# Optimization experiments

Measured on AMD Instinct MI355X. Metric: run time of the kernel, lower is better.

The kernel has to match this reference:

```python
import jax, jax.numpy as jnp
import numpy as np

NEG = -1e8


def lstm_scan(x, lens, Wih, Whh, b):
    # x: [B,S,D], lens: [B] int. PyTorch gate order i,f,g,o. Returns [B,S,H], zero at pad.
    B, S, D = x.shape
    H = Whh.shape[1]
    xs = jnp.swapaxes(x, 0, 1)  # [S,B,D]
    ts = jnp.arange(S)

    def step(carry, inp):
        h, c = carry
        xt, t = inp
        gates = xt @ Wih.T + h @ Whh.T + b  # [B,4H]
        i, f, g, o = jnp.split(gates, 4, axis=-1)
        i, f, o = jax.nn.sigmoid(i), jax.nn.sigmoid(f), jax.nn.sigmoid(o)
        g = jnp.tanh(g)
        c_new = f * c + i * g
        h_new = o * jnp.tanh(c_new)
        valid = (t < lens)[:, None]
        h = jnp.where(valid, h_new, h)
        c = jnp.where(valid, c_new, c)
        out = jnp.where(valid, h_new, 0.0)
        return (h, c), out

    init = (jnp.zeros((B, H), x.dtype), jnp.zeros((B, H), x.dtype))
    _, outs = jax.lax.scan(step, init, (xs, ts))
    return jnp.swapaxes(outs, 0, 1)  # [B,S,H]


def bilstm(x, lens, Wih_f, Whh_f, b_f, Wih_b, Whh_b, b_b):
    # forward direction
    out_f = lstm_scan(x, lens, Wih_f, Whh_f, b_f)
    # backward: reverse the valid prefix per sample (packed-sequence semantics)
    S = x.shape[1]
    t = jnp.arange(S)[None, :]
    idx = jnp.where(t < lens[:, None], lens[:, None] - 1 - t, t)  # [B,S]
    xr = jnp.take_along_axis(x, idx[:, :, None], axis=1)
    out_r = lstm_scan(xr, lens, Wih_b, Whh_b, b_b)
    out_b = jnp.take_along_axis(out_r, idx[:, :, None], axis=1)
    return jnp.concatenate([out_f, out_b], axis=-1)


def tnet_forward(seqs_id, seqs_len, asps_len, asps_mask, sent_mask,
                 embed, Wih_f, Whh_f, b_f, Wih_b, Whh_b, b_b,
                 W_cpt, b_cpt, W_as, b_as, Wq, bq, Wk, bk, Wv, bv, Wd, bd):
    seqs = embed[seqs_id]                                   # [B,S,D] (dropout = eval identity)
    seqs_lstm = bilstm(seqs, seqs_len, Wih_f, Whh_f, b_f, Wih_b, Whh_b, b_b)  # [B,S,D]

    # ragged aspect gather + pad + mean == masked mean (asps_mask==0 marks aspect tokens)
    asp_sel = (asps_mask == 0).astype(seqs_lstm.dtype)       # [B,S]
    asps = (seqs_lstm * asp_sel[:, :, None]).sum(axis=1) / asps_len[:, None].astype(seqs_lstm.dtype)
    asps = asps[:, None, :]                                  # [B,1,D]

    # CPT layers (flag='AS'); Attentions = dot-product attn, out = softmax(QK^T + mask) @ K
    x = seqs_lstm
    for _ in range(2):
        score = jax.nn.softmax(jnp.einsum('bqd,bkd->bqk', x, seqs_lstm) + asps_mask[:, None, :], axis=-1)
        attn_out = jnp.einsum('bqk,bkd->bqd', score, seqs_lstm)
        combine = jnp.concatenate([attn_out, x], axis=-1)    # [B,S,2D]
        linear_out = jax.nn.relu(combine @ W_cpt.T + b_cpt)
        scale = jax.nn.sigmoid(x @ W_as.T + b_as)
        x = scale * linear_out + (1.0 - scale) * x

    # QKVAttention over sentence
    D = x.shape[-1]
    Qp = asps @ Wq.T + bq                                    # [B,1,D]
    Kp = x @ Wk.T + bk                                       # [B,S,D]
    Vp = x @ Wv.T + bv
    sc = jax.nn.softmax(jnp.einsum('bqd,bkd->bqk', Qp, Kp) / jnp.sqrt(jnp.asarray(D, x.dtype))
                        + sent_mask[:, None, :], axis=-1)    # [B,1,S]
    out = jnp.einsum('bqk,bkd->bqd', sc, Vp)                 # [B,1,D]
    logits = out[:, 0] @ Wd.T + bd                           # [B,n_class]
    return logits, sc[:, 0]


def setup_inputs() -> dict:
    B, S, V, D, H, NC = 64, 256, 30000, 512, 256, 3
    key = jax.random.key(0)
    ks = jax.random.split(key, 24)

    seqs_id = jax.random.randint(ks[0], (B, S), 0, V)
    seqs_len = jax.random.randint(ks[1], (B,), S // 2, S + 1)
    asps_len = jax.random.randint(ks[2], (B,), 1, 6)
    start = jax.random.randint(ks[3], (B,), 0, S // 2 - 8)   # aspect span inside valid prefix
    pos = jnp.arange(S)[None, :]
    in_span = (pos >= start[:, None]) & (pos < (start + asps_len)[:, None])
    asps_mask = jnp.where(in_span, 0.0, NEG).astype(jnp.float32)
    sent_mask = jnp.where(pos < seqs_len[:, None], 0.0, NEG).astype(jnp.float32)

    def nrm(k, shape, s=0.02):
        return (s * jax.random.normal(k, shape)).astype(jnp.float32)

    inp = dict(seqs_id=seqs_id, seqs_len=seqs_len, asps_len=asps_len,
               asps_mask=asps_mask, sent_mask=sent_mask,
               embed=nrm(ks[4], (V, D), 0.1),
               Wih_f=nrm(ks[5], (4 * H, D)), Whh_f=nrm(ks[6], (4 * H, H)), b_f=jnp.zeros((4 * H,), jnp.float32),
               Wih_b=nrm(ks[7], (4 * H, D)), Whh_b=nrm(ks[8], (4 * H, H)), b_b=jnp.zeros((4 * H,), jnp.float32),
               W_cpt=nrm(ks[9], (D, 2 * D)), b_cpt=jnp.zeros((D,), jnp.float32),
               W_as=nrm(ks[10], (D, D)), b_as=jnp.zeros((D,), jnp.float32),
               Wq=nrm(ks[11], (D, D)), bq=jnp.zeros((D,), jnp.float32),
               Wk=nrm(ks[12], (D, D)), bk=jnp.zeros((D,), jnp.float32),
               Wv=nrm(ks[13], (D, D)), bv=jnp.zeros((D,), jnp.float32),
               Wd=nrm(ks[14], (NC, D)), bd=jnp.zeros((NC,), jnp.float32))
    return inp


def reference(seqs_id, seqs_len, asps_len, asps_mask, sent_mask,
              embed, Wih_f, Whh_f, b_f, Wih_b, Whh_b, b_b,
              W_cpt, b_cpt, W_as, b_as, Wq, bq, Wk, bk, Wv, bv, Wd, bd):
    return tnet_forward(seqs_id, seqs_len, asps_len, asps_mask, sent_mask,
                        embed, Wih_f, Whh_f, b_f, Wih_b, Whh_b, b_b,
                        W_cpt, b_cpt, W_as, b_as, Wq, bq, Wk, bk, Wv, bv, Wd, bd)
```

## Files before the change

### kernel.cpp

```cpp
#include <hip/hip_runtime.h>
#include <math.h>

constexpr int B_ = 64, S_ = 256, D_ = 512, H_ = 256, NC_ = 3;
constexpr int BS = B_ * S_;
constexpr int G4 = 4 * H_;

typedef __attribute__((ext_vector_type(4))) float f32x4;
typedef __attribute__((ext_vector_type(8))) short s16x8;
typedef unsigned short u16;
typedef unsigned long long u64;

template<int ACT>
static __device__ __forceinline__ float activate(float v) {
  if constexpr (ACT == 1) return v > 0.f ? v : 0.f;
  else if constexpr (ACT == 2) return 1.f / (1.f + expf(-v));
  else return v;
}

static __device__ __forceinline__ u16 f2bf_rne(float f) {
  unsigned u = __float_as_uint(f);
  return (u16)((u + 0x7FFFu + ((u >> 16) & 1u)) >> 16);
}
static __device__ __forceinline__ float bf2f(u16 h) {
  return __uint_as_float(((unsigned)h) << 16);
}
static __device__ __forceinline__ void splitf(float f, u16& h, u16& l) {
  h = f2bf_rne(f);
  float r = f - bf2f(h);
  l = f2bf_rne(r);
}

__global__ __launch_bounds__(256) void split_w(
    const float* __restrict__ src, u16* __restrict__ h, u16* __restrict__ l, int n4)
{
  int i = blockIdx.x * 256 + threadIdx.x;
  if (i >= n4) return;
  float4 v = ((const float4*)src)[i];
  ushort4 hh, ll;
  splitf(v.x, hh.x, ll.x); splitf(v.y, hh.y, ll.y);
  splitf(v.z, hh.z, ll.z); splitf(v.w, hh.w, ll.w);
  ((ushort4*)h)[i] = hh;
  ((ushort4*)l)[i] = ll;
}

__global__ __launch_bounds__(256) void gather_split(
    const float* __restrict__ embed, const int* __restrict__ gidx,
    u16* __restrict__ h, u16* __restrict__ l)
{
  int i = blockIdx.x * 256 + threadIdx.x;
  if (i >= BS * D_ / 4) return;
  int r = i >> 7;
  int c = (i & 127) << 2;
  float4 v = *(const float4*)(embed + (size_t)gidx[r] * D_ + c);
  ushort4 hh, ll;
  splitf(v.x, hh.x, ll.x); splitf(v.y, hh.y, ll.y);
  splitf(v.z, hh.z, ll.z); splitf(v.w, hh.w, ll.w);
  ((ushort4*)h)[i] = hh;
  ((ushort4*)l)[i] = ll;
}

template<int ACT, bool BT, bool ADDC, bool ASPL, bool BSPL, bool OSPL>
__global__ __launch_bounds__(256) void mgemm(
    const float* __restrict__ Af, const u16* __restrict__ Ah, const u16* __restrict__ Al,
    const float* __restrict__ Bf, const u16* __restrict__ Bh, const u16* __restrict__ Bl,
    const float* __restrict__ bias, const float* __restrict__ Cin,
    float* __restrict__ Co, u16* __restrict__ Oh, u16* __restrict__ Ol,
    int M, int N, int K, int ldb, long sA, long sB, long sC)
{
  __shared__ u16 AH[128][40];
  __shared__ u16 AL[128][40];
  __shared__ u16 BH[128][40];
  __shared__ u16 BL[128][40];

  const int tid = threadIdx.x;
  const int w = tid >> 6, l = tid & 63;
  const int m0 = blockIdx.x * 128, n0 = blockIdx.y * 128;
  const long zA = (long)blockIdx.z * sA;
  const long zB = (long)blockIdx.z * sB;
  const long zC = (long)blockIdx.z * sC;

  f32x4 acc[2][8];
  #pragma unroll
  for (int i = 0; i < 2; ++i)
    #pragma unroll
    for (int j = 0; j < 8; ++j) acc[i][j] = (f32x4){0.f, 0.f, 0.f, 0.f};

  const int ar = tid >> 1, ahh = tid & 1;
  const int bk = tid >> 3, bnq = tid & 7;
  const int lr = l & 15, lk = (l >> 4) * 8;

  for (int kt = 0; kt < K; kt += 32) {
    {
      int m = m0 + ar;
      if constexpr (ASPL) {
        s16x8 h0 = (s16x8)0, h1 = (s16x8)0, l0 = (s16x8)0, l1 = (s16x8)0;
        if (m < M) {
          const u16* ph = Ah + zA + (size_t)m * K + kt + ahh * 16;
          const u16* pl = Al + zA + (size_t)m * K + kt + ahh * 16;
          h0 = *(const s16x8*)ph; h1 = *(const s16x8*)(ph + 8);
          l0 = *(const s16x8*)pl; l1 = *(const s16x8*)(pl + 8);
        }
        *(s16x8*)&AH[ar][ahh * 16] = h0; *(s16x8*)&AH[ar][ahh * 16 + 8] = h1;
        *(s16x8*)&AL[ar][ahh * 16] = l0; *(s16x8*)&AL[ar][ahh * 16 + 8] = l1;
      } else {
        float vv[16];
        if (m < M) {
          const float* pf = Af + zA + (size_t)m * K + kt + ahh * 16;
          #pragma unroll
          for (int c = 0; c < 4; ++c) {
            float4 v = ((const float4*)pf)[c];
            vv[c * 4] = v.x; vv[c * 4 + 1] = v.y; vv[c * 4 + 2] = v.z; vv[c * 4 + 3] = v.w;
          }
        } else {
          #pragma unroll
          for (int c = 0; c < 16; ++c) vv[c] = 0.f;
        }
        u16 hh[16], ll[16];
        #pragma unroll
        for (int c = 0; c < 16; ++c) splitf(vv[c], hh[c], ll[c]);
        *(s16x8*)&AH[ar][ahh * 16] = *(s16x8*)&hh[0];
        *(s16x8*)&AH[ar][ahh * 16 + 8] = *(s16x8*)&hh[8];
        *(s16x8*)&AL[ar][ahh * 16] = *(s16x8*)&ll[0];
        *(s16x8*)&AL[ar][ahh * 16 + 8] = *(s16x8*)&ll[8];
      }
    }
    if constexpr (BT) {
      if constexpr (BSPL) {
        const u16* ph = Bh + zB + (size_t)(n0 + ar) * ldb + kt + ahh * 16;
        const u16* pl = Bl + zB + (size_t)(n0 + ar) * ldb + kt + ahh * 16;
        *(s16x8*)&BH[ar][ahh * 16] = *(const s16x8*)ph;
        *(s16x8*)&BH[ar][ahh * 16 + 8] = *(const s16x8*)(ph + 8);
        *(s16x8*)&BL[ar][ahh * 16] = *(const s16x8*)pl;
        *(s16x8*)&BL[ar][ahh * 16 + 8] = *(const s16x8*)(pl + 8);
      } else {
        const float* pf = Bf + zB + (size_t)(n0 + ar) * ldb + kt + ahh * 16;
        float vv[16];
        #pragma unroll
        for (int c = 0; c < 4; ++c) {
          float4 v = ((const float4*)pf)[c];
          vv[c * 4] = v.x; vv[c * 4 + 1] = v.y; vv[c * 4 + 2] = v.z; vv[c * 4 + 3] = v.w;
        }
        u16 hh[16], ll[16];
        #pragma unroll
        for (int c = 0; c < 16; ++c) splitf(vv[c], hh[c], ll[c]);
        *(s16x8*)&BH[ar][ahh * 16] = *(s16x8*)&hh[0];
        *(s16x8*)&BH[ar][ahh * 16 + 8] = *(s16x8*)&hh[8];
        *(s16x8*)&BL[ar][ahh * 16] = *(s16x8*)&ll[0];
        *(s16x8*)&BL[ar][ahh * 16 + 8] = *(s16x8*)&ll[8];
      }
    } else {
      const u16* ph = Bh + zB + (size_t)(kt + bk) * ldb + n0 + bnq * 16;
      const u16* pl = Bl + zB + (size_t)(kt + bk) * ldb + n0 + bnq * 16;
      s16x8 h8a = *(const s16x8*)ph, h8b = *(const s16x8*)(ph + 8);
      s16x8 l8a = *(const s16x8*)pl, l8b = *(const s16x8*)(pl + 8);
      #pragma unroll
      for (int jj = 0; jj < 8; ++jj) {
        BH[bnq * 16 + jj][bk] = (u16)h8a[jj];
        BH[bnq * 16 + 8 + jj][bk] = (u16)h8b[jj];
        BL[bnq * 16 + jj][bk] = (u16)l8a[jj];
        BL[bnq * 16 + 8 + jj][bk] = (u16)l8b[jj];
      }
    }
    __syncthreads();

    s16x8 afh[2], afl[2];
    #pragma unroll
    for (int i = 0; i < 2; ++i) {
      afh[i] = *(const s16x8*)&AH[w * 32 + i * 16 + lr][lk];
      afl[i] = *(const s16x8*)&AL[w * 32 + i * 16 + lr][lk];
    }
    #pragma unroll
    for (int j = 0; j < 8; ++j) {
      s16x8 bfh = *(const s16x8*)&BH[j * 16 + lr][lk];
      s16x8 bfl = *(const s16x8*)&BL[j * 16 + lr][lk];
      #pragma unroll
      for (int i = 0; i < 2; ++i) {
        acc[i][j] = __builtin_amdgcn_mfma_f32_16x16x32_bf16(afl[i], bfh, acc[i][j], 0, 0, 0);
        acc[i][j] = __builtin_amdgcn_mfma_f32_16x16x32_bf16(afh[i], bfl, acc[i][j], 0, 0, 0);
        acc[i][j] = __builtin_amdgcn_mfma_f32_16x16x32_bf16(afh[i], bfh, acc[i][j], 0, 0, 0);
      }
    }
    __syncthreads();
  }

  const int rl = (l >> 4) * 4;
  #pragma unroll
  for (int j = 0; j < 8; ++j) {
    int n = n0 + j * 16 + lr;
    float bv = bias ? bias[n] : 0.f;
    #pragma unroll
    for (int i = 0; i < 2; ++i) {
      #pragma unroll
      for (int e = 0; e < 4; ++e) {
        int m = m0 + w * 32 + i * 16 + rl + e;
        if (m < M) {
          float v = acc[i][j][e] + bv;
          if constexpr (ADDC) v += Cin[zC + (size_t)m * N + n];
          v = activate<ACT>(v);
          if constexpr (OSPL) {
            u16 hh, ll; splitf(v, hh, ll);
            Oh[zC + (size_t)m * N + n] = hh;
            Ol[zC + (size_t)m * N + n] = ll;
          } else {
            Co[zC + (size_t)m * N + n] = v;
          }
        }
      }
    }
  }
}

__global__ __launch_bounds__(256) void wf_prep(
    const float* __restrict__ Wf, const float* __restrict__ Wb, u16* __restrict__ WF)
{
  int gid = blockIdx.x * 256 + threadIdx.x;
  int lane = gid & 63;
  int nt = (gid >> 6) & 1;
  int kt = (gid >> 7) & 7;
  int w  = (gid >> 10) & 3;
  int j  = (gid >> 12) & 7;
  int dir = gid >> 15;
  const float* W = dir ? Wb : Wf;
  int r = w * 256 + j * 32 + nt * 16 + (lane & 15);
  int kb = kt * 32 + (lane >> 4) * 8;
  const float* src = W + (size_t)r * H_ + kb;
  u16 hh[8], ll[8];
  #pragma unroll
  for (int c = 0; c < 2; ++c) {
    float4 v = ((const float4*)src)[c];
    splitf(v.x, hh[c*4+0], ll[c*4+0]); splitf(v.y, hh[c*4+1], ll[c*4+1]);
    splitf(v.z, hh[c*4+2], ll[c*4+2]); splitf(v.w, hh[c*4+3], ll[c*4+3]);
  }
  size_t off = (size_t)(gid >> 6) * 1024 + (size_t)lane * 8;
  *(s16x8*)(WF + off)       = *(s16x8*)&hh[0];
  *(s16x8*)(WF + off + 512) = *(s16x8*)&ll[0];
}

__global__ __launch_bounds__(256) void zero_cnt(int* __restrict__ cnt)
{
  int i = blockIdx.x * 256 + threadIdx.x;
  if (i < 8 * 256) cnt[i] = 0;
}

__global__ __launch_bounds__(256, 1) void lstm_dist(
    const float* __restrict__ GX, const u16* __restrict__ WF,
    const int* __restrict__ lens, u16* __restrict__ outH, u16* __restrict__ outL,
    u64* __restrict__ ring64, int* __restrict__ cnt)
{
  const int bid = blockIdx.x;
  const int grp = bid & 7;
  const int j   = bid >> 3;
  const int dir = grp >> 2;
  const int bg  = grp & 3;
  const int b0g = bg * 16;
  const int tid = threadIdx.x;
  const int w = tid >> 6, l = tid & 63;

  const float* gx = GX + (size_t)dir * ((size_t)BS * G4);

  __shared__ int slen[16];
  __shared__ __align__(16) u16 AHs[16][264];
  __shared__ __align__(16) u16 ALs[16][264];
  __shared__ float act[4][16][32];
  if (tid < 16) slen[tid] = lens[b0g + tid];
  __syncthreads();

  s16x8 wh[8][2], wl[8][2];
  #pragma unroll
  for (int kt = 0; kt < 8; ++kt)
    #pragma unroll
    for (int nt = 0; nt < 2; ++nt) {
      size_t q = ((size_t)(((dir * 8 + j) * 4 + w) * 8 + kt) * 2 + nt);
      const u16* p = WF + q * 1024 + (size_t)l * 8;
      wh[kt][nt] = *(const s16x8*)p;
      wl[kt][nt] = *(const s16x8*)(p + 512);
    }

  const int ub = tid >> 4;
  const int uu = (tid & 15) * 2;
  const int len_b = slen[ub];
  float c0s = 0.f, c1s = 0.f, h0s = 0.f, h1s = 0.f;

  int* myCnt = cnt + grp * 256;
  const int lr = l & 15, lkb = (l >> 4) * 8;

  for (int t = 0; t < S_; ++t) {
    float gxv[2][4];
    #pragma unroll
    for (int nt = 0; nt < 2; ++nt)
      #pragma unroll
      for (int e = 0; e < 4; ++e) {
        int b = (l >> 4) * 4 + e;
        int len = slen[b];
        int pos = dir ? (t < len ? len - 1 - t : t) : t;
        gxv[nt][e] = gx[(size_t)((b0g + b) * S_ + pos) * G4 + (w * 256 + j * 32 + nt * 16 + lr)];
      }

    f32x4 acc[2];
    acc[0] = (f32x4){0.f, 0.f, 0.f, 0.f};
    acc[1] = (f32x4){0.f, 0.f, 0.f, 0.f};

    if (t > 0) {
      while (__hip_atomic_load(&myCnt[t - 1], __ATOMIC_RELAXED, __HIP_MEMORY_SCOPE_AGENT) < 32)
        __builtin_amdgcn_s_sleep(1);
      const int slot = (t - 1) & 3;
      const u64* rb = ring64 + ((size_t)slot * 8 + grp) * (16 * 128);
      u64 v[8];
      #pragma unroll
      for (int k = 0; k < 8; ++k)
        v[k] = __hip_atomic_load(&rb[k * 256 + tid], __ATOMIC_RELAXED, __HIP_MEMORY_SCOPE_AGENT);
      #pragma unroll
      for (int k = 0; k < 8; ++k) {
        int idx = k * 256 + tid;
        int b = idx >> 7, p = idx & 127;
        ushort4 q4 = *(ushort4*)&v[k];
        *(unsigned*)&AHs[b][2 * p] = (unsigned)q4.x | ((unsigned)q4.z << 16);
        *(unsigned*)&ALs[b][2 * p] = (unsigned)q4.y | ((unsigned)q4.w << 16);
      }
      __syncthreads();
      #pragma unroll
      for (int kt = 0; kt < 8; ++kt) {
        s16x8 ah = *(const s16x8*)&AHs[lr][kt * 32 + lkb];
        s16x8 al = *(const s16x8*)&ALs[lr][kt * 32 + lkb];
        #pragma unroll
        for (int nt = 0; nt < 2; ++nt) {
          acc[nt] = __builtin_amdgcn_mfma_f32_16x16x32_bf16(al, wh[kt][nt], acc[nt], 0, 0, 0);
          acc[nt] = __builtin_amdgcn_mfma_f32_16x16x32_bf16(ah, wl[kt][nt], acc[nt], 0, 0, 0);
          acc[nt] = __builtin_amdgcn_mfma_f32_16x16x32_bf16(ah, wh[kt][nt], acc[nt], 0, 0, 0);
        }
      }
    }

    #pragma unroll
    for (int nt = 0; nt < 2; ++nt)
      #pragma unroll
      for (int e = 0; e < 4; ++e) {
        float v = acc[nt][e] + gxv[nt][e];
        v = (w == 2) ? tanhf(v) : 1.f / (1.f + expf(-v));
        act[w][(l >> 4) * 4 + e][nt * 16 + lr] = v;
      }
    __syncthreads();

    {
      int pos = dir ? (t < len_b ? len_b - 1 - t : t) : t;
      bool valid = t < len_b;
      float i0 = act[0][ub][uu],     f0 = act[1][ub][uu],     g0 = act[2][ub][uu],     o0 = act[3][ub][uu];
      float i1 = act[0][ub][uu + 1], f1 = act[1][ub][uu + 1], g1 = act[2][ub][uu + 1], o1 = act[3][ub][uu + 1];
      float cn0 = fmaf(f0, c0s, i0 * g0), cn1 = fmaf(f1, c1s, i1 * g1);
      float hn0 = o0 * tanhf(cn0), hn1 = o1 * tanhf(cn1);
      if (valid) { c0s = cn0; h0s = hn0; c1s = cn1; h1s = hn1; }
      ushort4 pk;
      splitf(h0s, pk.x, pk.y); splitf(h1s, pk.z, pk.w);
      const int slot = t & 3;
      size_t ridx = ((size_t)slot * 8 + grp) * (16 * 128) + (size_t)ub * 128 + (j * 32 + uu) / 2;
      __hip_atomic_store(&ring64[ridx], *(u64*)&pk, __ATOMIC_RELAXED, __HIP_MEMORY_SCOPE_AGENT);
      asm volatile("s_waitcnt vmcnt(0)" ::: "memory");
      if (l == 0)
        __hip_atomic_fetch_add(&myCnt[t], 1, __ATOMIC_RELAXED, __HIP_MEMORY_SCOPE_AGENT);
      float ov0 = valid ? hn0 : 0.f, ov1 = valid ? hn1 : 0.f;
      u16 oh0, qq0, oh1, qq1;
      splitf(ov0, oh0, qq0); splitf(ov1, oh1, qq1);
      size_t obase = (size_t)((b0g + ub) * S_ + pos) * (2 * H_) + dir * H_ + j * 32 + uu;
      *(ushort2*)&outH[obase] = make_ushort2(oh0, oh1);
      *(ushort2*)&outL[obase] = make_ushort2(qq0, qq1);
    }
    __syncthreads();
  }
}

__global__ __launch_bounds__(512) void asps_k(
    const u16* __restrict__ lh, const u16* __restrict__ ll,
    const float* __restrict__ amask, const int* __restrict__ alen, float* __restrict__ asps)
{
  int b = blockIdx.x, d = threadIdx.x;
  float acc = 0.f;
  for (int t = 0; t < S_; ++t)
    if (amask[b * S_ + t] == 0.f) {
      size_t i = ((size_t)(b * S_ + t)) * D_ + d;
      acc += bf2f(lh[i]) + bf2f(ll[i]);
    }
  asps[b * D_ + d] = acc / (float)alen[b];
}

__global__ __launch_bounds__(256) void softmax_rows(
    const float* __restrict__ p_, const float* __restrict__ mask,
    u16* __restrict__ ph, u16* __restrict__ pl)
{
  const int row = blockIdx.x;
  const int b = row >> 8;
  const int tid = threadIdx.x;
  const float* p = p_ + (size_t)row * S_;
  float v = p[tid] + mask[(b << 8) | tid];
  float m = v;
  #pragma unroll
  for (int off = 32; off > 0; off >>= 1) m = fmaxf(m, __shfl_xor(m, off));
  __shared__ float r1[4];
  __shared__ float r2[4];
  const int w = tid >> 6, l = tid & 63;
  if (l == 0) r1[w] = m;
  __syncthreads();
  m = fmaxf(fmaxf(r1[0], r1[1]), fmaxf(r1[2], r1[3]));
  float e = expf(v - m);
  float s = e;
  #pragma unroll
  for (int off = 32; off > 0; off >>= 1) s += __shfl_xor(s, off);
  if (l == 0) r2[w] = s;
  __syncthreads();
  s = r2[0] + r2[1] + r2[2] + r2[3];
  float o = e / s;
  u16 hh, ll; splitf(o, hh, ll);
  ph[(size_t)row * S_ + tid] = hh;
  pl[(size_t)row * S_ + tid] = ll;
}

__global__ __launch_bounds__(256) void xupdate(
    const u16* __restrict__ xh, const u16* __restrict__ xl,
    const float4* __restrict__ sc, const float4* __restrict__ lin,
    u16* __restrict__ oh, u16* __restrict__ ol, int n4)
{
  int i = blockIdx.x * 256 + threadIdx.x;
  if (i >= n4) return;
  ushort4 h4 = ((const ushort4*)xh)[i];
  ushort4 l4 = ((const ushort4*)xl)[i];
  float4 s = sc[i], lv = lin[i];
  float x0 = bf2f(h4.x) + bf2f(l4.x);
  float x1 = bf2f(h4.y) + bf2f(l4.y);
  float x2 = bf2f(h4.z) + bf2f(l4.z);
  float x3 = bf2f(h4.w) + bf2f(l4.w);
  float o0 = s.x * lv.x + (1.f - s.x) * x0;
  float o1 = s.y * lv.y + (1.f - s.y) * x1;
  float o2 = s.z * lv.z + (1.f - s.z) * x2;
  float o3 = s.w * lv.w + (1.f - s.w) * x3;
  ushort4 hh, ll;
  splitf(o0, hh.x, ll.x); splitf(o1, hh.y, ll.y);
  splitf(o2, hh.z, ll.z); splitf(o3, hh.w, ll.w);
  ((ushort4*)oh)[i] = hh;
  ((ushort4*)ol)[i] = ll;
}

__global__ __launch_bounds__(256) void final_sc_k(
    const float* __restrict__ Qp, const float* __restrict__ Kp,
    const float* __restrict__ smask, float* __restrict__ outsc)
{
  int b = blockIdx.x, tid = threadIdx.x;
  __shared__ float q[D_];
  q[tid] = Qp[b * D_ + tid];
  q[tid + 256] = Qp[b * D_ + tid + 256];
  __syncthreads();
  const float4* kr = (const float4*)(Kp + ((size_t)(b * S_ + tid)) * D_);
  float acc = 0.f;
  #pragma unroll 4
  for (int d = 0; d < D_ / 4; ++d) {
    float4 kv = kr[d];
    acc += q[4 * d] * kv.x + q[4 * d + 1] * kv.y + q[4 * d + 2] * kv.z + q[4 * d + 3] * kv.w;
  }
  float v = acc / sqrtf((float)D_) + smask[b * S_ + tid];
  float m = v;
  #pragma unroll
  for (int off = 32; off > 0; off >>= 1) m = fmaxf(m, __shfl_xor(m, off));
  __shared__ float r1[4];
  __shared__ float r2[4];
  const int w = tid >> 6, l = tid & 63;
  if (l == 0) r1[w] = m;
  __syncthreads();
  m = fmaxf(fmaxf(r1[0], r1[1]), fmaxf(r1[2], r1[3]));
  float e = expf(v - m);
  float s = e;
  #pragma unroll
  for (int off = 32; off > 0; off >>= 1) s += __shfl_xor(s, off);
  if (l == 0) r2[w] = s;
  __syncthreads();
  s = r2[0] + r2[1] + r2[2] + r2[3];
  outsc[b * S_ + tid] = e / s;
}

__global__ __launch_bounds__(512) void out_vec_k(
    const float* __restrict__ sc, const float* __restrict__ Vp, float* __restrict__ outv)
{
  int b = blockIdx.x, d = threadIdx.x;
  __shared__ float s[S_];
  if (d < S_) s[d] = sc[b * S_ + d];
  __syncthreads();
  float acc = 0.f;
  for (int k = 0; k < S_; ++k) acc = fmaf(s[k], Vp[((size_t)(b * S_ + k)) * D_ + d], acc);
  outv[b * D_ + d] = acc;
}

__global__ __launch_bounds__(192) void logits_k(
    const float* __restrict__ outv, const float* __restrict__ Wd,
    const float* __restrict__ bd, float* __restrict__ out)
{
  int b = blockIdx.x;
  int c = threadIdx.x >> 6, l = threadIdx.x & 63;
  float acc = 0.f;
  for (int d = l; d < D_; d += 64) acc = fmaf(outv[b * D_ + d], Wd[c * D_ + d], acc);
  #pragma unroll
  for (int off = 32; off > 0; off >>= 1) acc += __shfl_down(acc, off);
  if (l == 0) out[b * NC_ + c] = acc + bd[c];
}

extern "C" void kernel_launch(void* const* d_in, const int* in_sizes, int n_in,
                              void* d_out, int out_size, void* d_ws, size_t ws_size,
                              hipStream_t stream)
{
  const int*   seqs_id   = (const int*)d_in[0];
  const int*   seqs_len  = (const int*)d_in[1];
  const int*   asps_len  = (const int*)d_in[2];
  const float* asps_mask = (const float*)d_in[3];
  const float* sent_mask = (const float*)d_in[4];
  const float* embed     = (const float*)d_in[5];
  const float* Wih_f     = (const float*)d_in[6];
  const float* Whh_f     = (const float*)d_in[7];
  const float* b_f       = (const float*)d_in[8];
  const float* Wih_b     = (const float*)d_in[9];
  const float* Whh_b     = (const float*)d_in[10];
  const float* b_b       = (const float*)d_in[11];
  const float* W_cpt     = (const float*)d_in[12];
  const float* b_cpt     = (const float*)d_in[13];
  const float* W_as      = (const float*)d_in[14];
  const float* b_as      = (const float*)d_in[15];
  const float* Wq        = (const float*)d_in[16];
  const float* bq        = (const float*)d_in[17];
  const float* Wk        = (const float*)d_in[18];
  const float* bk        = (const float*)d_in[19];
  const float* Wv        = (const float*)d_in[20];
  const float* bv        = (const float*)d_in[21];
  const float* Wd        = (const float*)d_in[22];
  const float* bd        = (const float*)d_in[23];

  float* w = (float*)d_ws;
  size_t off = 0;
  auto alloc = [&](size_t words) { size_t o = off; off += words; return o; };
  struct Split { u16* h; u16* l; };
  auto salloc = [&](size_t n) {
    size_t o = alloc(n);
    Split s; s.h = (u16*)(w + o); s.l = (u16*)(w + o) + n; return s;
  };

  const size_t off_wf   = alloc(524288);
  const size_t off_ring = alloc(131072);
  const size_t off_cnt  = alloc(2048);
  Split sWihF = salloc(4ul * H_ * D_);
  Split sWihB = salloc(4ul * H_ * D_);
  Split sWcpt = salloc((size_t)D_ * 2 * D_);
  Split sWas  = salloc((size_t)D_ * D_);
  Split sWk   = salloc((size_t)D_ * D_);
  Split sWv   = salloc((size_t)D_ * D_);
  Split sWq   = salloc((size_t)D_ * D_);
  Split sLstm = salloc((size_t)BS * D_);
  const size_t off_asps = alloc((size_t)B_ * D_);
  const size_t off_qp   = alloc((size_t)B_ * D_);
  const size_t off_outv = alloc((size_t)B_ * D_);
  Split sAsps = salloc((size_t)B_ * D_);

  const size_t dyn0 = off;
  Split sXemb; sXemb.h = (u16*)(w + dyn0); sXemb.l = sXemb.h + (size_t)BS * D_;
  float* GX = w + dyn0 + (size_t)BS * D_;
  size_t p2 = dyn0;
  float* scoreF = w + p2;                 p2 += (size_t)B_ * S_ * S_;
  Split sScore; sScore.h = (u16*)(w + p2); sScore.l = sScore.h + (size_t)B_ * S_ * S_; p2 += (size_t)B_ * S_ * S_;
  Split sAttn;  sAttn.h  = (u16*)(w + p2); sAttn.l  = sAttn.h + (size_t)BS * D_;       p2 += (size_t)BS * D_;
  float* lin = w + p2;                    p2 += (size_t)BS * D_;
  float* scl = w + p2;                    p2 += (size_t)BS * D_;
  Split sX;     sX.h     = (u16*)(w + p2); sX.l     = sX.h + (size_t)BS * D_;           p2 += (size_t)BS * D_;

  u16* WF      = (u16*)(w + off_wf);
  u64* ring64  = (u64*)(w + off_ring);
  int* cnt     = (int*)(w + off_cnt);
  float* aspsb = w + off_asps;
  float* qp    = w + off_qp;
  float* outv  = w + off_outv;
  float* Kp    = (float*)sAttn.h;
  float* Vp    = lin;
  float* logits = (float*)d_out;
  float* outsc  = (float*)d_out + B_ * NC_;

  zero_cnt<<<8, 256, 0, stream>>>(cnt);
  wf_prep<<<256, 256, 0, stream>>>(Whh_f, Whh_b, WF);
  split_w<<<512, 256, 0, stream>>>(Wih_f, sWihF.h, sWihF.l, H_ * D_);
  split_w<<<512, 256, 0, stream>>>(Wih_b, sWihB.h, sWihB.l, H_ * D_);
  split_w<<<512, 256, 0, stream>>>(W_cpt, sWcpt.h, sWcpt.l, D_ * 2 * D_ / 4);
  split_w<<<256, 256, 0, stream>>>(W_as, sWas.h, sWas.l, D_ * D_ / 4);
  split_w<<<256, 256, 0, stream>>>(Wk, sWk.h, sWk.l, D_ * D_ / 4);
  split_w<<<256, 256, 0, stream>>>(Wv, sWv.h, sWv.l, D_ * D_ / 4);
  split_w<<<256, 256, 0, stream>>>(Wq, sWq.h, sWq.l, D_ * D_ / 4);
  gather_split<<<BS * D_ / 4 / 256, 256, 0, stream>>>(embed, seqs_id, sXemb.h, sXemb.l);

  mgemm<0, true, false, true, true, false><<<dim3(128, 8, 1), 256, 0, stream>>>(
      nullptr, sXemb.h, sXemb.l, nullptr, sWihF.h, sWihF.l, b_f, nullptr,
      GX, nullptr, nullptr, BS, G4, D_, D_, 0, 0, 0);
  mgemm<0, true, false, true, true, false><<<dim3(128, 8, 1), 256, 0, stream>>>(
      nullptr, sXemb.h, sXemb.l, nullptr, sWihB.h, sWihB.l, b_b, nullptr,
      GX + (size_t)BS * G4, nullptr, nullptr, BS, G4, D_, D_, 0, 0, 0);

  lstm_dist<<<64, 256, 0, stream>>>(GX, WF, seqs_len, sLstm.h, sLstm.l, ring64, cnt);
  asps_k<<<B_, D_, 0, stream>>>(sLstm.h, sLstm.l, asps_mask, asps_len, aspsb);

  for (int it = 0; it < 2; ++it) {
    const Split xin = (it == 0) ? sLstm : sX;
    mgemm<0, true, false, true, true, false><<<dim3(2, 2, B_), 256, 0, stream>>>(
        nullptr, xin.h, xin.l, nullptr, sLstm.h, sLstm.l, nullptr, nullptr,
        scoreF, nullptr, nullptr, S_, S_, D_, D_,
        (long)S_ * D_, (long)S_ * D_, (long)S_ * S_);
    softmax_rows<<<BS, 256, 0, stream>>>(scoreF, asps_mask, sScore.h, sScore.l);
    mgemm<0, false, false, true, true, true><<<dim3(2, 4, B_), 256, 0, stream>>>(
        nullptr, sScore.h, sScore.l, nullptr, sLstm.h, sLstm.l, nullptr, nullptr,
        nullptr, sAttn.h, sAttn.l, S_, D_, S_, D_,
        (long)S_ * S_, (long)S_ * D_, (long)S_ * D_);
    mgemm<0, true, false, true, true, false><<<dim3(128, 4, 1), 256, 0, stream>>>(
        nullptr, sAttn.h, sAttn.l, nullptr, sWcpt.h, sWcpt.l, b_cpt, nullptr,
        lin, nullptr, nullptr, BS, D_, D_, 2 * D_, 0, 0, 0);
    mgemm<1, true, true, true, true, false><<<dim3(128, 4, 1), 256, 0, stream>>>(
        nullptr, xin.h, xin.l, nullptr, sWcpt.h + D_, sWcpt.l + D_, nullptr, lin,
        lin, nullptr, nullptr, BS, D_, D_, 2 * D_, 0, 0, 0);
    mgemm<2, true, false, true, true, false><<<dim3(128, 4, 1), 256, 0, stream>>>(
        nullptr, xin.h, xin.l, nullptr, sWas.h, sWas.l, b_as, nullptr,
        scl, nullptr, nullptr, BS, D_, D_, D_, 0, 0, 0);
    xupdate<<<(BS * D_ / 4 + 255) / 256, 256, 0, stream>>>(
        xin.h, xin.l, (const float4*)scl, (const float4*)lin, sX.h, sX.l, BS * D_ / 4);
  }

  mgemm<0, true, false, true, true, false><<<dim3(128, 4, 1), 256, 0, stream>>>(
      nullptr, sX.h, sX.l, nullptr, sWk.h, sWk.l, bk, nullptr,
      Kp, nullptr, nullptr, BS, D_, D_, D_, 0, 0, 0);
  mgemm<0, true, false, true, true, false><<<dim3(128, 4, 1), 256, 0, stream>>>(
      nullptr, sX.h, sX.l, nullptr, sWv.h, sWv.l, bv, nullptr,
      Vp, nullptr, nullptr, BS, D_, D_, D_, 0, 0, 0);
  mgemm<0, true, false, false, true, false><<<dim3(1, 4, 1), 256, 0, stream>>>(
      aspsb, nullptr, nullptr, nullptr, sWq.h, sWq.l, bq, nullptr,
      qp, nullptr, nullptr, B_, D_, D_, D_, 0, 0, 0);

  final_sc_k<<<B_, 256, 0, stream>>>(qp, Kp, sent_mask, outsc);
  out_vec_k<<<B_, D_, 0, stream>>>(outsc, Vp, outv);
  logits_k<<<B_, 192, 0, stream>>>(outv, Wd, bd, logits);
}
```

Before: 1.596 ms.

## Replace counter barrier in distributed LSTM with generation-tagged ring flags

Drops the per-step atomic counter and its spin-wait in the cross-block LSTM recurrence. Each ring entry now carries a 2-bit generation tag in the low mantissa bits of the fp32 h value, and consumers poll their own entries until the tag matches. This removes the vmcnt wait, the fetch_add and one block barrier per step, and double-buffers the activation scratch to make that safe. The price is that h is exchanged as fp32 with its 2 low mantissa bits lost, and each step pays for re-splitting into bf16 hi/lo on the consumer side.

```diff
diff --git a/kernel.cpp b/kernel.cpp
--- a/kernel.cpp
+++ b/kernel.cpp
@@ -236,16 +236,16 @@
   *(s16x8*)(WF + off + 512) = *(s16x8*)&ll[0];
 }
 
-__global__ __launch_bounds__(256) void zero_cnt(int* __restrict__ cnt)
+__global__ __launch_bounds__(256) void ring_init(u64* __restrict__ ring64)
 {
   int i = blockIdx.x * 256 + threadIdx.x;
-  if (i < 8 * 256) cnt[i] = 0;
+  __hip_atomic_store(&ring64[i], (u64)3, __ATOMIC_RELAXED, __HIP_MEMORY_SCOPE_AGENT);
 }
 
 __global__ __launch_bounds__(256, 1) void lstm_dist(
     const float* __restrict__ GX, const u16* __restrict__ WF,
     const int* __restrict__ lens, u16* __restrict__ outH, u16* __restrict__ outL,
-    u64* __restrict__ ring64, int* __restrict__ cnt)
+    u64* __restrict__ ring64)
 {
   const int bid = blockIdx.x;
   const int grp = bid & 7;
@@ -261,7 +261,7 @@
   __shared__ int slen[16];
   __shared__ __align__(16) u16 AHs[16][264];
   __shared__ __align__(16) u16 ALs[16][264];
-  __shared__ float act[4][16][32];
+  __shared__ float act[2][4][16][33];
   if (tid < 16) slen[tid] = lens[b0g + tid];
   __syncthreads();
 
@@ -281,7 +281,6 @@
   const int len_b = slen[ub];
   float c0s = 0.f, c1s = 0.f, h0s = 0.f, h1s = 0.f;
 
-  int* myCnt = cnt + grp * 256;
   const int lr = l & 15, lkb = (l >> 4) * 8;
 
   for (int t = 0; t < S_; ++t) {
@@ -301,21 +300,32 @@
     acc[1] = (f32x4){0.f, 0.f, 0.f, 0.f};
 
     if (t > 0) {
-      while (__hip_atomic_load(&myCnt[t - 1], __ATOMIC_RELAXED, __HIP_MEMORY_SCOPE_AGENT) < 32)
-        __builtin_amdgcn_s_sleep(1);
+      const unsigned gen = (unsigned)(((t - 1) >> 2) & 3);
       const int slot = (t - 1) & 3;
-      const u64* rb = ring64 + ((size_t)slot * 8 + grp) * (16 * 128);
+      u64* rb = ring64 + ((size_t)slot * 8 + grp) * (16 * 128);
       u64 v[8];
-      #pragma unroll
-      for (int k = 0; k < 8; ++k)
-        v[k] = __hip_atomic_load(&rb[k * 256 + tid], __ATOMIC_RELAXED, __HIP_MEMORY_SCOPE_AGENT);
+      unsigned need = 0xFFu;
+      do {
+        unsigned nn = 0;
+        #pragma unroll
+        for (int k = 0; k < 8; ++k)
+          if ((need >> k) & 1)
+            v[k] = __hip_atomic_load(&rb[k * 256 + tid], __ATOMIC_RELAXED, __HIP_MEMORY_SCOPE_AGENT);
+        #pragma unroll
+        for (int k = 0; k < 8; ++k)
+          if (((need >> k) & 1) && ((unsigned)v[k] & 3u) != gen) nn |= 1u << k;
+        need = nn;
+      } while (need);
       #pragma unroll
       for (int k = 0; k < 8; ++k) {
         int idx = k * 256 + tid;
         int b = idx >> 7, p = idx & 127;
-        ushort4 q4 = *(ushort4*)&v[k];
-        *(unsigned*)&AHs[b][2 * p] = (unsigned)q4.x | ((unsigned)q4.z << 16);
-        *(unsigned*)&ALs[b][2 * p] = (unsigned)q4.y | ((unsigned)q4.w << 16);
+        float f0 = __uint_as_float((unsigned)v[k] & ~3u);
+        float f1 = __uint_as_float((unsigned)(v[k] >> 32));
+        u16 hh0, ll0, hh1, ll1;
+        splitf(f0, hh0, ll0); splitf(f1, hh1, ll1);
+        *(unsigned*)&AHs[b][2 * p] = (unsigned)hh0 | ((unsigned)hh1 << 16);
+        *(unsigned*)&ALs[b][2 * p] = (unsigned)ll0 | ((unsigned)ll1 << 16);
       }
       __syncthreads();
       #pragma unroll
@@ -331,32 +341,32 @@
       }
     }
 
+    const int pb = t & 1;
     #pragma unroll
     for (int nt = 0; nt < 2; ++nt)
       #pragma unroll
       for (int e = 0; e < 4; ++e) {
         float v = acc[nt][e] + gxv[nt][e];
         v = (w == 2) ? tanhf(v) : 1.f / (1.f + expf(-v));
-        act[w][(l >> 4) * 4 + e][nt * 16 + lr] = v;
+        act[pb][w][(l >> 4) * 4 + e][nt * 16 + lr] = v;
       }
     __syncthreads();
 
     {
       int pos = dir ? (t < len_b ? len_b - 1 - t : t) : t;
       bool valid = t < len_b;
-      float i0 = act[0][ub][uu],     f0 = act[1][ub][uu],     g0 = act[2][ub][uu],     o0 = act[3][ub][uu];
-      float i1 = act[0][ub][uu + 1], f1 = act[1][ub][uu + 1], g1 = act[2][ub][uu + 1], o1 = act[3][ub][uu + 1];
+      float i0 = act[pb][0][ub][uu],     f0 = act[pb][1][ub][uu],     g0 = act[pb][2][ub][uu],     o0 = act[pb][3][ub][uu];
+      float i1 = act[pb][0][ub][uu + 1], f1 = act[pb][1][ub][uu + 1], g1 = act[pb][2][ub][uu + 1], o1 = act[pb][3][ub][uu + 1];
       float cn0 = fmaf(f0, c0s, i0 * g0), cn1 = fmaf(f1, c1s, i1 * g1);
       float hn0 = o0 * tanhf(cn0), hn1 = o1 * tanhf(cn1);
       if (valid) { c0s = cn0; h0s = hn0; c1s = cn1; h1s = hn1; }
-      ushort4 pk;
-      splitf(h0s, pk.x, pk.y); splitf(h1s, pk.z, pk.w);
+      unsigned gen = (unsigned)((t >> 2) & 3);
+      unsigned a0 = (__float_as_uint(h0s) & ~3u) | gen;
+      unsigned a1 = __float_as_uint(h1s);
+      u64 word = ((u64)a1 << 32) | (u64)a0;
       const int slot = t & 3;
-      size_t ridx = ((size_t)slot * 8 + grp) * (16 * 128) + (size_t)ub * 128 + (j * 32 + uu) / 2;
-      __hip_atomic_store(&ring64[ridx], *(u64*)&pk, __ATOMIC_RELAXED, __HIP_MEMORY_SCOPE_AGENT);
-      asm volatile("s_waitcnt vmcnt(0)" ::: "memory");
-      if (l == 0)
-        __hip_atomic_fetch_add(&myCnt[t], 1, __ATOMIC_RELAXED, __HIP_MEMORY_SCOPE_AGENT);
+      size_t ridx = ((size_t)slot * 8 + grp) * (16 * 128) + (size_t)ub * 128 + j * 16 + (tid & 15);
+      __hip_atomic_store(&ring64[ridx], word, __ATOMIC_RELAXED, __HIP_MEMORY_SCOPE_AGENT);
       float ov0 = valid ? hn0 : 0.f, ov1 = valid ? hn1 : 0.f;
       u16 oh0, qq0, oh1, qq1;
       splitf(ov0, oh0, qq0); splitf(ov1, oh1, qq1);
@@ -364,7 +374,6 @@
       *(ushort2*)&outH[obase] = make_ushort2(oh0, oh1);
       *(ushort2*)&outL[obase] = make_ushort2(qq0, qq1);
     }
-    __syncthreads();
   }
 }
 
@@ -539,7 +548,6 @@
 
   const size_t off_wf   = alloc(524288);
   const size_t off_ring = alloc(131072);
-  const size_t off_cnt  = alloc(2048);
   Split sWihF = salloc(4ul * H_ * D_);
   Split sWihB = salloc(4ul * H_ * D_);
   Split sWcpt = salloc((size_t)D_ * 2 * D_);
@@ -551,7 +559,6 @@
   const size_t off_asps = alloc((size_t)B_ * D_);
   const size_t off_qp   = alloc((size_t)B_ * D_);
   const size_t off_outv = alloc((size_t)B_ * D_);
-  Split sAsps = salloc((size_t)B_ * D_);
 
   const size_t dyn0 = off;
   Split sXemb; sXemb.h = (u16*)(w + dyn0); sXemb.l = sXemb.h + (size_t)BS * D_;
@@ -566,7 +573,6 @@
 
   u16* WF      = (u16*)(w + off_wf);
   u64* ring64  = (u64*)(w + off_ring);
-  int* cnt     = (int*)(w + off_cnt);
   float* aspsb = w + off_asps;
   float* qp    = w + off_qp;
   float* outv  = w + off_outv;
@@ -575,7 +581,7 @@
   float* logits = (float*)d_out;
   float* outsc  = (float*)d_out + B_ * NC_;
 
-  zero_cnt<<<8, 256, 0, stream>>>(cnt);
+  ring_init<<<256, 256, 0, stream>>>(ring64);
   wf_prep<<<256, 256, 0, stream>>>(Whh_f, Whh_b, WF);
   split_w<<<512, 256, 0, stream>>>(Wih_f, sWihF.h, sWihF.l, H_ * D_);
   split_w<<<512, 256, 0, stream>>>(Wih_b, sWihB.h, sWihB.l, H_ * D_);
@@ -593,7 +599,7 @@
       nullptr, sXemb.h, sXemb.l, nullptr, sWihB.h, sWihB.l, b_b, nullptr,
       GX + (size_t)BS * G4, nullptr, nullptr, BS, G4, D_, D_, 0, 0, 0);
 
-  lstm_dist<<<64, 256, 0, stream>>>(GX, WF, seqs_len, sLstm.h, sLstm.l, ring64, cnt);
+  lstm_dist<<<64, 256, 0, stream>>>(GX, WF, seqs_len, sLstm.h, sLstm.l, ring64);
   asps_k<<<B_, D_, 0, stream>>>(sLstm.h, sLstm.l, asps_mask, asps_len, aspsb);
 
   for (int it = 0; it < 2; ++it) {
```

New measurement: 1.587 ms. About the same (-0.6%).
